# Optimization experiments

Hardware: AMD Instinct MI355X
Metric: run time of the kernel (lower is better)

Reference implementation:

```python
import jax, jax.numpy as jnp
import numpy as np

N, E, H, G, L = 100000, 200000, 32, 100, 4
NODE_IN, EDGE_IN, NGRAPH = 6, 4, 50
EPS = 1e-5

def setup_inputs() -> dict:
    key = jax.random.key(0)
    ks = jax.random.split(key, 32)
    s = 0.05
    inp = {
        "x": jax.random.normal(ks[0], (N, NODE_IN), jnp.float32),
        "edge_index": jax.random.randint(ks[1], (2, E), 0, N, jnp.int64),
        "edge_attr": jax.random.normal(ks[2], (E, EDGE_IN), jnp.float32),
        "batch": jnp.sort(jax.random.randint(ks[3], (N,), 0, NGRAPH, jnp.int64)),
        # node embedding: Linear + ReLU + BatchNorm1d
        "w_embed": jax.random.normal(ks[4], (NODE_IN, H), jnp.float32) * s,
        "b_embed": jnp.zeros((H,), jnp.float32),
        "bn_gamma": jnp.ones((H,), jnp.float32),
        "bn_beta": jnp.zeros((H,), jnp.float32),
        # NNConv layers (stacked over L): edge MLP Linear(EDGE_IN,2H)->ReLU->Linear(2H,H*H), root weight, bias
        "conv_w1": jax.random.normal(ks[5], (L, EDGE_IN, 2 * H), jnp.float32) * s,
        "conv_b1": jnp.zeros((L, 2 * H), jnp.float32),
        "conv_w2": jax.random.normal(ks[6], (L, 2 * H, H * H), jnp.float32) * s,
        "conv_b2": jnp.zeros((L, H * H), jnp.float32),
        "conv_root": jax.random.normal(ks[7], (L, H, H), jnp.float32) * s,
        "conv_bias": jnp.zeros((L, H), jnp.float32),
        # heads
        "wk_w1": jax.random.normal(ks[8], (H, H), jnp.float32) * s,
        "wk_b1": jnp.zeros((H,), jnp.float32),
        "wk_w2": jax.random.normal(ks[9], (H, 1), jnp.float32) * s,
        "wk_b2": jnp.zeros((1,), jnp.float32),
        "uj_w1": jax.random.normal(ks[10], (H, H), jnp.float32) * s,
        "uj_b1": jnp.zeros((H,), jnp.float32),
        "uj_w2": jax.random.normal(ks[11], (H, G), jnp.float32) * s,
        "uj_b2": jnp.zeros((G,), jnp.float32),
        "zk_w1": jax.random.normal(ks[12], (H, H), jnp.float32) * s,
        "zk_b1": jnp.zeros((H,), jnp.float32),
        "zk_w2": jax.random.normal(ks[13], (H, G), jnp.float32) * s,
        "zk_b2": jnp.zeros((G,), jnp.float32),
    }
    return inp

def _mlp2(h, w1, b1, w2, b2):
    return jax.nn.relu(h @ w1 + b1) @ w2 + b2

def _forward(x, edge_index, edge_attr, batch,
             w_embed, b_embed, bn_gamma, bn_beta,
             conv_w1, conv_b1, conv_w2, conv_b2, conv_root, conv_bias,
             wk_w1, wk_b1, wk_w2, wk_b2,
             uj_w1, uj_b1, uj_w2, uj_b2,
             zk_w1, zk_b1, zk_w2, zk_b2):
    src, dst = edge_index[0], edge_index[1]
    # node embed: Linear -> ReLU -> BatchNorm1d (training-mode batch stats)
    h = jax.nn.relu(x @ w_embed + b_embed)
    mu = h.mean(axis=0)
    var = ((h - mu) ** 2).mean(axis=0)  # biased, as torch BN uses for normalization
    h = (h - mu) * jax.lax.rsqrt(var + EPS) * bn_gamma + bn_beta
    # in-degree for mean aggregation
    deg = jax.ops.segment_sum(jnp.ones((E,), h.dtype), dst, num_segments=N)
    inv_deg = (1.0 / jnp.maximum(deg, 1.0))[:, None]
    for l in range(L):
        # per-edge weight matrix from edge MLP: [E, H, H]
        W = _mlp2(edge_attr, conv_w1[l], conv_b1[l], conv_w2[l], conv_b2[l]).reshape(E, H, H)
        msg = jnp.einsum('ei,eio->eo', h[src], W)  # gather + per-edge matmul
        agg = jax.ops.segment_sum(msg, dst, num_segments=N) * inv_deg  # scatter-mean
        h = jax.nn.relu(agg + h @ conv_root[l] + conv_bias[l])
    # global mean pool over graphs
    cnt = jax.ops.segment_sum(jnp.ones((N,), h.dtype), batch, num_segments=NGRAPH)
    hg = jax.ops.segment_sum(h, batch, num_segments=NGRAPH) / jnp.maximum(cnt, 1.0)[:, None]
    wk = _mlp2(hg, wk_w1, wk_b1, wk_w2, wk_b2).squeeze(-1)
    uj = _mlp2(hg, uj_w1, uj_b1, uj_w2, uj_b2)
    zk = _mlp2(hg, zk_w1, zk_b1, zk_w2, zk_b2)
    return wk, uj, zk

def reference(x, edge_index, edge_attr, batch,
              w_embed, b_embed, bn_gamma, bn_beta,
              conv_w1, conv_b1, conv_w2, conv_b2, conv_root, conv_bias,
              wk_w1, wk_b1, wk_w2, wk_b2,
              uj_w1, uj_b1, uj_w2, uj_b2,
              zk_w1, zk_b1, zk_w2, zk_b2):
    return _forward(x, edge_index, edge_attr, batch,
                    w_embed, b_embed, bn_gamma, bn_beta,
                    conv_w1, conv_b1, conv_w2, conv_b2, conv_root, conv_bias,
                    wk_w1, wk_b1, wk_w2, wk_b2,
                    uj_w1, uj_b1, uj_w2, uj_b2,
                    zk_w1, zk_b1, zk_w2, zk_b2)
```

## Files before the change

kernel.cpp:

```cpp
#include <hip/hip_runtime.h>

#define NN 100000
#define NE 200000
#define HH 32
#define NL 4
#define NGR 50
#define GOUT 100
#define NODE_IN 6
#define NEB 782

typedef __attribute__((ext_vector_type(8))) short bf16x8;
typedef __attribute__((ext_vector_type(4))) float f32x4;

__device__ __forceinline__ unsigned short bf16_rne(float x) {
    unsigned int b = __float_as_uint(x);
    b += 0x7FFFu + ((b >> 16) & 1u);
    return (unsigned short)(b >> 16);
}
__device__ __forceinline__ float bf16_f(unsigned short h) {
    return __uint_as_float(((unsigned int)h) << 16);
}

__global__ __launch_bounds__(256) void split_w2(const float* __restrict__ w2,
                                                unsigned short* __restrict__ w2h,
                                                unsigned short* __restrict__ w2l)
{
    int id = blockIdx.x * 256 + threadIdx.x;
    if (id >= NL * 64 * 1024) return;
    int l = id >> 16, rem = id & 65535;
    int k = rem >> 10, n = rem & 1023;
    float v = w2[id];
    unsigned short hi = bf16_rne(v);
    float lov = v - bf16_f(hi);
    unsigned short lo = bf16_rne(lov);
    int out = l * 65536 + n * 64 + k;
    w2h[out] = hi;
    w2l[out] = lo;
}

__global__ __launch_bounds__(256) void embed_kernel(
    const float* __restrict__ x, const float* __restrict__ w,
    const float* __restrict__ b, float* __restrict__ h0)
{
    int nid = blockIdx.x * 256 + threadIdx.x;
    if (nid >= NN) return;
    float xv[NODE_IN];
    #pragma unroll
    for (int d = 0; d < NODE_IN; ++d) xv[d] = x[nid * NODE_IN + d];
    float4* op = (float4*)(h0 + (size_t)nid * HH);
    #pragma unroll
    for (int q = 0; q < 8; ++q) {
        float4 r;
        float* rp = (float*)&r;
        #pragma unroll
        for (int u = 0; u < 4; ++u) {
            int j = q * 4 + u;
            float a = b[j];
            #pragma unroll
            for (int d = 0; d < NODE_IN; ++d) a = fmaf(xv[d], w[d * HH + j], a);
            rp[u] = fmaxf(a, 0.f);
        }
        op[q] = r;
    }
}

__global__ __launch_bounds__(256) void stats_kernel(const float* __restrict__ h0,
                                                    float* __restrict__ stats)
{
    __shared__ float ls[64];
    int tid = threadIdx.x;
    if (tid < 64) ls[tid] = 0.f;
    __syncthreads();
    float s[4] = {0.f, 0.f, 0.f, 0.f};
    float q[4] = {0.f, 0.f, 0.f, 0.f};
    const float4* h4 = (const float4*)h0;
    const int total = NN * HH / 4;
    for (int idx = blockIdx.x * 256 + tid; idx < total; idx += 128 * 256) {
        float4 v = h4[idx];
        s[0] += v.x; q[0] += v.x * v.x;
        s[1] += v.y; q[1] += v.y * v.y;
        s[2] += v.z; q[2] += v.z * v.z;
        s[3] += v.w; q[3] += v.w * v.w;
    }
    int c0 = (tid * 4) & 31;
    #pragma unroll
    for (int u = 0; u < 4; ++u) {
        atomicAdd(&ls[c0 + u], s[u]);
        atomicAdd(&ls[32 + c0 + u], q[u]);
    }
    __syncthreads();
    if (tid < 64) unsafeAtomicAdd(&stats[tid], ls[tid]);
}

__global__ __launch_bounds__(256) void degi_kernel(const int* __restrict__ ei,
                                                   int* __restrict__ degi)
{
    int e = blockIdx.x * 256 + threadIdx.x;
    if (e >= NE) return;
    atomicAdd(&degi[ei[NE + e]], 1);
}

__global__ void bn_finalize(const float* __restrict__ stats,
                            const float* __restrict__ gamma,
                            const float* __restrict__ beta,
                            float* __restrict__ bnp)
{
    int j = threadIdx.x;
    if (j >= HH) return;
    const float invn = 1.0f / (float)NN;
    float mu  = stats[j] * invn;
    float var = stats[32 + j] * invn - mu * mu;
    float rs  = 1.0f / sqrtf(var + 1e-5f);
    float sc  = rs * gamma[j];
    bnp[j]      = sc;
    bnp[32 + j] = beta[j] - mu * sc;
}

__global__ __launch_bounds__(256) void bn_apply(float* __restrict__ h,
                                                const float* __restrict__ bnp)
{
    int idx = blockIdx.x * 256 + threadIdx.x;
    if (idx >= NN * HH / 4) return;
    float4 v = ((float4*)h)[idx];
    int j = (idx * 4) & 31;
    v.x = fmaf(v.x, bnp[j + 0], bnp[32 + j + 0]);
    v.y = fmaf(v.y, bnp[j + 1], bnp[32 + j + 1]);
    v.z = fmaf(v.z, bnp[j + 2], bnp[32 + j + 2]);
    v.w = fmaf(v.w, bnp[j + 3], bnp[32 + j + 3]);
    ((float4*)h)[idx] = v;
}

__global__ __launch_bounds__(256) void scan1(const int* __restrict__ degi,
                                             int* __restrict__ rowptr,
                                             int* __restrict__ bsum)
{
    __shared__ int sd[256];
    int tid = threadIdx.x;
    int i = blockIdx.x * 256 + tid;
    int v = (i < NN) ? degi[i] : 0;
    sd[tid] = v;
    __syncthreads();
    #pragma unroll
    for (int off = 1; off < 256; off <<= 1) {
        int t = (tid >= off) ? sd[tid - off] : 0;
        __syncthreads();
        sd[tid] += t;
        __syncthreads();
    }
    if (i < NN) rowptr[i] = sd[tid] - v;
    if (tid == 255) bsum[blockIdx.x] = sd[255];
}

__global__ __launch_bounds__(512) void scan2(int* __restrict__ bsum)
{
    __shared__ int sd[512];
    int tid = threadIdx.x;
    int v = (tid < 391) ? bsum[tid] : 0;
    sd[tid] = v;
    __syncthreads();
    #pragma unroll
    for (int off = 1; off < 512; off <<= 1) {
        int t = (tid >= off) ? sd[tid - off] : 0;
        __syncthreads();
        sd[tid] += t;
        __syncthreads();
    }
    if (tid < 391) bsum[tid] = sd[tid] - v;
}

__global__ __launch_bounds__(256) void scan3(int* __restrict__ rowptr,
                                             const int* __restrict__ bsum,
                                             int* __restrict__ cursor)
{
    int i = blockIdx.x * 256 + threadIdx.x;
    if (i < NN) {
        int r = rowptr[i] + bsum[blockIdx.x];
        rowptr[i] = r;
        cursor[i] = r;
    }
    if (i == 0) rowptr[NN] = NE;
}

__global__ __launch_bounds__(256) void scatter_k(const int* __restrict__ ei,
                                                 int* __restrict__ cursor,
                                                 int* __restrict__ perm)
{
    int e = blockIdx.x * 256 + threadIdx.x;
    if (e >= NE) return;
    int d = ei[NE + e];
    int pos = atomicAdd(&cursor[d], 1);
    perm[pos] = e;
}

__global__ __launch_bounds__(256) void edge_mfma(
    const float* __restrict__ h, const int* __restrict__ ei,
    const float* __restrict__ ea, const int* __restrict__ perm,
    const float* __restrict__ w1, const float* __restrict__ b1,
    const unsigned short* __restrict__ w2h, const unsigned short* __restrict__ w2l,
    const float* __restrict__ b2, float* __restrict__ msg)
{
    __shared__ float hT[32 * 256];
    __shared__ float b2l[1024];
    __shared__ unsigned short Bh[4096];
    __shared__ unsigned short Bl[4096];

    const int tid  = threadIdx.x;
    const int lane = tid & 63;
    const int l15  = lane & 15;
    const int lg   = lane >> 4;
    const int eb   = blockIdx.x * 256;
    const int wavebase = tid & ~63;

    const unsigned int* gh = (const unsigned int*)w2h;
    const unsigned int* gl = (const unsigned int*)w2l;

    auto stage = [&](int c2) {
        #pragma unroll
        for (int q = 0; q < 2; ++q) {
            int g = q * 256 + tid;
            int n = g >> 3, j = g & 7;
            int gi = ((c2 * 64 + n) << 3) + (j ^ (n & 7));
            int lb = (q * 256 + wavebase) * 8;
            __builtin_amdgcn_global_load_lds(
                (const __attribute__((address_space(1))) unsigned int*)(gh + (size_t)gi * 4),
                (__attribute__((address_space(3))) unsigned int*)(&Bh[0] + lb), 16, 0, 0);
            __builtin_amdgcn_global_load_lds(
                (const __attribute__((address_space(1))) unsigned int*)(gl + (size_t)gi * 4),
                (__attribute__((address_space(3))) unsigned int*)(&Bl[0] + lb), 16, 0, 0);
        }
    };

    {
        int e = eb + tid;
        int pe = (e < NE) ? perm[e] : 0;
        int s  = (e < NE) ? ei[pe] : 0;
        const float4* hp = (const float4*)(h + (size_t)s * HH);
        #pragma unroll
        for (int q = 0; q < 8; ++q) {
            float4 v = hp[q];
            hT[(q * 4 + 0) * 256 + tid] = v.x;
            hT[(q * 4 + 1) * 256 + tid] = v.y;
            hT[(q * 4 + 2) * 256 + tid] = v.z;
            hT[(q * 4 + 3) * 256 + tid] = v.w;
        }
        ((float4*)b2l)[tid] = ((const float4*)b2)[tid];
    }

    bf16x8 thi[4][2], tlo[4][2];
    #pragma unroll
    for (int et = 0; et < 4; ++et) {
        int e2 = eb + wavebase + et * 16 + l15;
        bool ev = (e2 < NE);
        int pe2 = ev ? perm[e2] : 0;
        float4 eav = make_float4(0.f, 0.f, 0.f, 0.f);
        if (ev) eav = *(const float4*)(ea + (size_t)pe2 * 4);
        #pragma unroll
        for (int ks = 0; ks < 2; ++ks) {
            int k0 = ks * 32 + lg * 8;
            #pragma unroll
            for (int j = 0; j < 8; ++j) {
                float t = b1[k0 + j];
                t = fmaf(eav.x, w1[0 * 64 + k0 + j], t);
                t = fmaf(eav.y, w1[1 * 64 + k0 + j], t);
                t = fmaf(eav.z, w1[2 * 64 + k0 + j], t);
                t = fmaf(eav.w, w1[3 * 64 + k0 + j], t);
                t = ev ? fmaxf(t, 0.f) : 0.f;
                unsigned short hi = bf16_rne(t);
                float lov = t - bf16_f(hi);
                unsigned short lo = bf16_rne(lov);
                thi[et][ks][j] = (short)hi;
                tlo[et][ks][j] = (short)lo;
            }
        }
    }

    float acc0[4][4], acc1[4][4];
    #pragma unroll
    for (int et = 0; et < 4; ++et)
        #pragma unroll
        for (int r = 0; r < 4; ++r) { acc0[et][r] = 0.f; acc1[et][r] = 0.f; }

    for (int c2 = 0; c2 < 16; ++c2) {
        __syncthreads();
        stage(c2);
        __syncthreads();

        #pragma unroll
        for (int ntp = 0; ntp < 2; ++ntp) {
            const int i = c2 * 2 + ntp;
            float4 h4[4];
            #pragma unroll
            for (int et = 0; et < 4; ++et)
                h4[et] = *(const float4*)&hT[i * 256 + wavebase + et * 16 + lg * 4];
            #pragma unroll
            for (int half = 0; half < 2; ++half) {
                int nt = ntp * 2 + half;
                int nl = nt * 16 + l15;
                int swz = (nl & 7) << 4;
                const char* bhrow = (const char*)&Bh[0] + nl * 128;
                const char* blrow = (const char*)&Bl[0] + nl * 128;
                bf16x8 Bh0 = *(const bf16x8*)(bhrow + (( 0 + lg * 16) ^ swz));
                bf16x8 Bl0 = *(const bf16x8*)(blrow + (( 0 + lg * 16) ^ swz));
                bf16x8 Bh1 = *(const bf16x8*)(bhrow + ((64 + lg * 16) ^ swz));
                bf16x8 Bl1 = *(const bf16x8*)(blrow + ((64 + lg * 16) ^ swz));
                float b2v = b2l[c2 * 64 + nt * 16 + l15];
                #pragma unroll
                for (int et = 0; et < 4; ++et) {
                    f32x4 G = {0.f, 0.f, 0.f, 0.f};
                    G = __builtin_amdgcn_mfma_f32_16x16x32_bf16(thi[et][0], Bh0, G, 0, 0, 0);
                    G = __builtin_amdgcn_mfma_f32_16x16x32_bf16(tlo[et][0], Bh0, G, 0, 0, 0);
                    G = __builtin_amdgcn_mfma_f32_16x16x32_bf16(thi[et][0], Bl0, G, 0, 0, 0);
                    G = __builtin_amdgcn_mfma_f32_16x16x32_bf16(thi[et][1], Bh1, G, 0, 0, 0);
                    G = __builtin_amdgcn_mfma_f32_16x16x32_bf16(tlo[et][1], Bh1, G, 0, 0, 0);
                    G = __builtin_amdgcn_mfma_f32_16x16x32_bf16(thi[et][1], Bl1, G, 0, 0, 0);
                    if (half == 0) {
                        acc0[et][0] = fmaf(h4[et].x, G[0] + b2v, acc0[et][0]);
                        acc0[et][1] = fmaf(h4[et].y, G[1] + b2v, acc0[et][1]);
                        acc0[et][2] = fmaf(h4[et].z, G[2] + b2v, acc0[et][2]);
                        acc0[et][3] = fmaf(h4[et].w, G[3] + b2v, acc0[et][3]);
                    } else {
                        acc1[et][0] = fmaf(h4[et].x, G[0] + b2v, acc1[et][0]);
                        acc1[et][1] = fmaf(h4[et].y, G[1] + b2v, acc1[et][1]);
                        acc1[et][2] = fmaf(h4[et].z, G[2] + b2v, acc1[et][2]);
                        acc1[et][3] = fmaf(h4[et].w, G[3] + b2v, acc1[et][3]);
                    }
                }
            }
        }
    }

    #pragma unroll
    for (int et = 0; et < 4; ++et) {
        #pragma unroll
        for (int r = 0; r < 4; ++r) {
            int row = eb + wavebase + et * 16 + lg * 4 + r;
            if (row < NE) {
                msg[(size_t)row * HH + l15]      = acc0[et][r];
                msg[(size_t)row * HH + 16 + l15] = acc1[et][r];
            }
        }
    }
}

__global__ __launch_bounds__(256) void node_kernel(
    const float* __restrict__ h, const float* __restrict__ msg,
    const int* __restrict__ rowptr, const float* __restrict__ root,
    const float* __restrict__ bias, float* __restrict__ hout)
{
    int nid = blockIdx.x * 256 + threadIdx.x;
    if (nid >= NN) return;
    int j0 = rowptr[nid], j1 = rowptr[nid + 1];
    float hv[HH];
    {
        const float4* hp = (const float4*)(h + (size_t)nid * HH);
        #pragma unroll
        for (int q = 0; q < 8; ++q) {
            float4 v = hp[q];
            hv[4*q+0] = v.x; hv[4*q+1] = v.y; hv[4*q+2] = v.z; hv[4*q+3] = v.w;
        }
    }
    float acc[HH];
    #pragma unroll
    for (int o = 0; o < HH; ++o) acc[o] = bias[o];
    #pragma unroll
    for (int i = 0; i < HH; ++i) {
        float hi = hv[i];
        #pragma unroll
        for (int o = 0; o < HH; ++o) acc[o] = fmaf(hi, root[i * HH + o], acc[o]);
    }
    float s[HH];
    #pragma unroll
    for (int o = 0; o < HH; ++o) s[o] = 0.f;
    for (int j = j0; j < j1; ++j) {
        const float4* mp = (const float4*)(msg + (size_t)j * HH);
        #pragma unroll
        for (int q = 0; q < 8; ++q) {
            float4 m = mp[q];
            s[4*q+0] += m.x; s[4*q+1] += m.y; s[4*q+2] += m.z; s[4*q+3] += m.w;
        }
    }
    float inv = 1.0f / fmaxf((float)(j1 - j0), 1.0f);
    float4* op = (float4*)(hout + (size_t)nid * HH);
    #pragma unroll
    for (int q = 0; q < 8; ++q) {
        float4 r;
        r.x = fmaxf(fmaf(s[4*q+0], inv, acc[4*q+0]), 0.f);
        r.y = fmaxf(fmaf(s[4*q+1], inv, acc[4*q+1]), 0.f);
        r.z = fmaxf(fmaf(s[4*q+2], inv, acc[4*q+2]), 0.f);
        r.w = fmaxf(fmaf(s[4*q+3], inv, acc[4*q+3]), 0.f);
        op[q] = r;
    }
}

__global__ __launch_bounds__(256) void pool_kernel(
    const float* __restrict__ h, const int* __restrict__ batch,
    float* __restrict__ pool, float* __restrict__ cnt)
{
    __shared__ float lp[NGR * HH];
    __shared__ float lc[NGR];
    int tid = threadIdx.x;
    for (int i = tid; i < NGR * HH; i += 256) lp[i] = 0.f;
    if (tid < NGR) lc[tid] = 0.f;
    __syncthreads();
    int c = tid & 31, grp = tid >> 5;
    int base = blockIdx.x * 1024 + grp * 128;
    int curg = -1;
    float acc = 0.f, cn = 0.f;
    for (int s = 0; s < 128; ++s) {
        int n = base + s;
        if (n >= NN) break;
        int g = batch[n];
        if (g != curg) {
            if (curg >= 0) {
                atomicAdd(&lp[curg * HH + c], acc);
                if (c == 0) atomicAdd(&lc[curg], cn);
            }
            curg = g; acc = 0.f; cn = 0.f;
        }
        acc += h[(size_t)n * HH + c];
        cn += 1.f;
    }
    if (curg >= 0) {
        atomicAdd(&lp[curg * HH + c], acc);
        if (c == 0) atomicAdd(&lc[curg], cn);
    }
    __syncthreads();
    for (int i = tid; i < NGR * HH; i += 256)
        if (lp[i] != 0.f) unsafeAtomicAdd(&pool[i], lp[i]);
    if (tid < NGR && lc[tid] != 0.f) unsafeAtomicAdd(&cnt[tid], lc[tid]);
}

__global__ __launch_bounds__(256) void heads_kernel(
    const float* __restrict__ pool, const float* __restrict__ cnt,
    const float* __restrict__ wkw1, const float* __restrict__ wkb1,
    const float* __restrict__ wkw2, const float* __restrict__ wkb2,
    const float* __restrict__ ujw1, const float* __restrict__ ujb1,
    const float* __restrict__ ujw2, const float* __restrict__ ujb2,
    const float* __restrict__ zkw1, const float* __restrict__ zkb1,
    const float* __restrict__ zkw2, const float* __restrict__ zkb2,
    float* __restrict__ out)
{
    __shared__ float hg[NGR * HH];
    __shared__ float hid[NGR * HH];
    int tid = threadIdx.x;
    int head = blockIdx.x;
    const float *w1, *b1, *w2, *b2;
    if (head == 0)      { w1 = wkw1; b1 = wkb1; w2 = wkw2; b2 = wkb2; }
    else if (head == 1) { w1 = ujw1; b1 = ujb1; w2 = ujw2; b2 = ujb2; }
    else                { w1 = zkw1; b1 = zkb1; w2 = zkw2; b2 = zkb2; }
    for (int i = tid; i < NGR * HH; i += 256) {
        int g = i >> 5;
        hg[i] = pool[i] / fmaxf(cnt[g], 1.0f);
    }
    __syncthreads();
    for (int i = tid; i < NGR * HH; i += 256) {
        int g = i >> 5, c = i & 31;
        float a = b1[c];
        for (int j = 0; j < HH; ++j) a = fmaf(hg[g * HH + j], w1[j * HH + c], a);
        hid[i] = fmaxf(a, 0.f);
    }
    __syncthreads();
    if (head == 0) {
        if (tid < NGR) {
            float a = b2[0];
            for (int c = 0; c < HH; ++c) a = fmaf(hid[tid * HH + c], w2[c], a);
            out[tid] = a;
        }
    } else {
        float* ob = out + NGR + (head - 1) * NGR * GOUT;
        for (int i = tid; i < NGR * GOUT; i += 256) {
            int g = i / GOUT, u = i % GOUT;
            float a = b2[u];
            for (int c = 0; c < HH; ++c) a = fmaf(hid[g * HH + c], w2[c * GOUT + u], a);
            ob[i] = a;
        }
    }
}

extern "C" void kernel_launch(void* const* d_in, const int* in_sizes, int n_in,
                              void* d_out, int out_size, void* d_ws, size_t ws_size,
                              hipStream_t stream)
{
    const float* x     = (const float*)d_in[0];
    const int*   ei    = (const int*)d_in[1];
    const float* ea    = (const float*)d_in[2];
    const int*   batch = (const int*)d_in[3];
    const float* w_emb = (const float*)d_in[4];
    const float* b_emb = (const float*)d_in[5];
    const float* gamma = (const float*)d_in[6];
    const float* beta  = (const float*)d_in[7];
    const float* cw1   = (const float*)d_in[8];
    const float* cb1   = (const float*)d_in[9];
    const float* cw2   = (const float*)d_in[10];
    const float* cb2   = (const float*)d_in[11];
    const float* croot = (const float*)d_in[12];
    const float* cbias = (const float*)d_in[13];
    float* out = (float*)d_out;

    unsigned short* w2h = (unsigned short*)d_ws;
    unsigned short* w2l = w2h + 262144;
    float* msg    = (float*)(w2l + 262144);
    float* h0     = msg + (size_t)NE * HH;
    float* h1     = h0 + (size_t)NN * HH;
    int*   rowptr = (int*)(h1 + (size_t)NN * HH);
    int*   cursor = rowptr + 100004;
    int*   perm   = cursor + NN;
    int*   degi   = perm + NE;
    int*   bsum   = degi + NN;
    float* stats  = (float*)(bsum + 512);
    float* pool   = stats + 64;
    float* cnt    = pool + NGR * HH;
    float* bnp    = cnt + NGR;

    hipMemsetAsync(degi, 0, (size_t)(NN + 512 + 64 + NGR * HH + NGR) * sizeof(int), stream);

    split_w2<<<(NL * 65536) / 256, 256, 0, stream>>>(cw2, w2h, w2l);
    embed_kernel<<<(NN + 255) / 256, 256, 0, stream>>>(x, w_emb, b_emb, h0);
    stats_kernel<<<128, 256, 0, stream>>>(h0, stats);
    degi_kernel<<<NEB, 256, 0, stream>>>(ei, degi);
    bn_finalize<<<1, 32, 0, stream>>>(stats, gamma, beta, bnp);
    bn_apply<<<(NN * HH / 4 + 255) / 256, 256, 0, stream>>>(h0, bnp);

    scan1<<<391, 256, 0, stream>>>(degi, rowptr, bsum);
    scan2<<<1, 512, 0, stream>>>(bsum);
    scan3<<<391, 256, 0, stream>>>(rowptr, bsum, cursor);
    scatter_k<<<NEB, 256, 0, stream>>>(ei, cursor, perm);

    float* hc = h0;
    float* hn = h1;
    for (int l = 0; l < NL; ++l) {
        edge_mfma<<<NEB, 256, 0, stream>>>(
            hc, ei, ea, perm,
            cw1 + (size_t)l * 4 * 64, cb1 + (size_t)l * 64,
            w2h + (size_t)l * 65536, w2l + (size_t)l * 65536,
            cb2 + (size_t)l * 1024, msg);
        node_kernel<<<(NN + 255) / 256, 256, 0, stream>>>(
            hc, msg, rowptr, croot + (size_t)l * HH * HH, cbias + (size_t)l * HH, hn);
        float* t = hc; hc = hn; hn = t;
    }

    pool_kernel<<<(NN + 1023) / 1024, 256, 0, stream>>>(hc, batch, pool, cnt);
    heads_kernel<<<3, 256, 0, stream>>>(pool, cnt,
        (const float*)d_in[14], (const float*)d_in[15], (const float*)d_in[16], (const float*)d_in[17],
        (const float*)d_in[18], (const float*)d_in[19], (const float*)d_in[20], (const float*)d_in[21],
        (const float*)d_in[22], (const float*)d_in[23], (const float*)d_in[24], (const float*)d_in[25],
        out);
}
```

Measured before the change: 773.6 us.

## Load edge-MLP weights directly into registers with double-buffered prefetch

Drops the LDS staging of the split bf16 W2 tiles and the two barriers per chunk. Each wave now reads its B fragments straight from global memory (L2-resident) into registers, using a two-deep register ping-pong so loads for the next column group overlap the MFMAs of the current one. This removes barrier stalls and LDS traffic. The cost is more registers, redundant global/L2 reads across waves, and uncoalesced 16-byte loads per lane.

```diff
diff --git a/kernel.cpp b/kernel.cpp
--- a/kernel.cpp
+++ b/kernel.cpp
@@ -192,6 +192,55 @@
     perm[pos] = e;
 }
 
+#define LOADB(S, ii)                                                              \
+    {                                                                             \
+        const size_t r0 = (size_t)((ii) * 32 + l15) * 64;                         \
+        const size_t r1 = r0 + 16 * 64;                                           \
+        S##h0a = *(const bf16x8*)(wh + r0);                                       \
+        S##h0b = *(const bf16x8*)(wh + r0 + 32);                                  \
+        S##h1a = *(const bf16x8*)(wh + r1);                                       \
+        S##h1b = *(const bf16x8*)(wh + r1 + 32);                                  \
+        S##l0a = *(const bf16x8*)(wl + r0);                                       \
+        S##l0b = *(const bf16x8*)(wl + r0 + 32);                                  \
+        S##l1a = *(const bf16x8*)(wl + r1);                                       \
+        S##l1b = *(const bf16x8*)(wl + r1 + 32);                                  \
+    }
+
+#define COMPUTE(S, ii)                                                            \
+    {                                                                             \
+        float4 h4[4];                                                             \
+        _Pragma("unroll")                                                         \
+        for (int et = 0; et < 4; ++et)                                            \
+            h4[et] = *(const float4*)&hT[(ii) * 256 + wavebase + et * 16 + lg * 4];\
+        float b2v0 = b2l[(ii) * 32 + l15];                                        \
+        float b2v1 = b2l[(ii) * 32 + 16 + l15];                                   \
+        _Pragma("unroll")                                                         \
+        for (int et = 0; et < 4; ++et) {                                          \
+            f32x4 G = {0.f, 0.f, 0.f, 0.f};                                       \
+            G = __builtin_amdgcn_mfma_f32_16x16x32_bf16(thi[et][0], S##h0a, G, 0, 0, 0); \
+            G = __builtin_amdgcn_mfma_f32_16x16x32_bf16(tlo[et][0], S##h0a, G, 0, 0, 0); \
+            G = __builtin_amdgcn_mfma_f32_16x16x32_bf16(thi[et][0], S##l0a, G, 0, 0, 0); \
+            G = __builtin_amdgcn_mfma_f32_16x16x32_bf16(thi[et][1], S##h0b, G, 0, 0, 0); \
+            G = __builtin_amdgcn_mfma_f32_16x16x32_bf16(tlo[et][1], S##h0b, G, 0, 0, 0); \
+            G = __builtin_amdgcn_mfma_f32_16x16x32_bf16(thi[et][1], S##l0b, G, 0, 0, 0); \
+            acc0[et][0] = fmaf(h4[et].x, G[0] + b2v0, acc0[et][0]);               \
+            acc0[et][1] = fmaf(h4[et].y, G[1] + b2v0, acc0[et][1]);               \
+            acc0[et][2] = fmaf(h4[et].z, G[2] + b2v0, acc0[et][2]);               \
+            acc0[et][3] = fmaf(h4[et].w, G[3] + b2v0, acc0[et][3]);               \
+            f32x4 H = {0.f, 0.f, 0.f, 0.f};                                       \
+            H = __builtin_amdgcn_mfma_f32_16x16x32_bf16(thi[et][0], S##h1a, H, 0, 0, 0); \
+            H = __builtin_amdgcn_mfma_f32_16x16x32_bf16(tlo[et][0], S##h1a, H, 0, 0, 0); \
+            H = __builtin_amdgcn_mfma_f32_16x16x32_bf16(thi[et][0], S##l1a, H, 0, 0, 0); \
+            H = __builtin_amdgcn_mfma_f32_16x16x32_bf16(thi[et][1], S##h1b, H, 0, 0, 0); \
+            H = __builtin_amdgcn_mfma_f32_16x16x32_bf16(tlo[et][1], S##h1b, H, 0, 0, 0); \
+            H = __builtin_amdgcn_mfma_f32_16x16x32_bf16(thi[et][1], S##l1b, H, 0, 0, 0); \
+            acc1[et][0] = fmaf(h4[et].x, H[0] + b2v1, acc1[et][0]);               \
+            acc1[et][1] = fmaf(h4[et].y, H[1] + b2v1, acc1[et][1]);               \
+            acc1[et][2] = fmaf(h4[et].z, H[2] + b2v1, acc1[et][2]);               \
+            acc1[et][3] = fmaf(h4[et].w, H[3] + b2v1, acc1[et][3]);               \
+        }                                                                         \
+    }
+
 __global__ __launch_bounds__(256) void edge_mfma(
     const float* __restrict__ h, const int* __restrict__ ei,
     const float* __restrict__ ea, const int* __restrict__ perm,
@@ -201,8 +250,6 @@
 {
     __shared__ float hT[32 * 256];
     __shared__ float b2l[1024];
-    __shared__ unsigned short Bh[4096];
-    __shared__ unsigned short Bl[4096];
 
     const int tid  = threadIdx.x;
     const int lane = tid & 63;
@@ -211,24 +258,8 @@
     const int eb   = blockIdx.x * 256;
     const int wavebase = tid & ~63;
 
-    const unsigned int* gh = (const unsigned int*)w2h;
-    const unsigned int* gl = (const unsigned int*)w2l;
-
-    auto stage = [&](int c2) {
-        #pragma unroll
-        for (int q = 0; q < 2; ++q) {
-            int g = q * 256 + tid;
-            int n = g >> 3, j = g & 7;
-            int gi = ((c2 * 64 + n) << 3) + (j ^ (n & 7));
-            int lb = (q * 256 + wavebase) * 8;
-            __builtin_amdgcn_global_load_lds(
-                (const __attribute__((address_space(1))) unsigned int*)(gh + (size_t)gi * 4),
-                (__attribute__((address_space(3))) unsigned int*)(&Bh[0] + lb), 16, 0, 0);
-            __builtin_amdgcn_global_load_lds(
-                (const __attribute__((address_space(1))) unsigned int*)(gl + (size_t)gi * 4),
-                (__attribute__((address_space(3))) unsigned int*)(&Bl[0] + lb), 16, 0, 0);
-        }
-    };
+    const unsigned short* __restrict__ wh = w2h + lg * 8;
+    const unsigned short* __restrict__ wl = w2l + lg * 8;
 
     {
         int e = eb + tid;
@@ -280,54 +311,20 @@
         #pragma unroll
         for (int r = 0; r < 4; ++r) { acc0[et][r] = 0.f; acc1[et][r] = 0.f; }
 
-    for (int c2 = 0; c2 < 16; ++c2) {
-        __syncthreads();
-        stage(c2);
-        __syncthreads();
-
-        #pragma unroll
-        for (int ntp = 0; ntp < 2; ++ntp) {
-            const int i = c2 * 2 + ntp;
-            float4 h4[4];
-            #pragma unroll
-            for (int et = 0; et < 4; ++et)
-                h4[et] = *(const float4*)&hT[i * 256 + wavebase + et * 16 + lg * 4];
-            #pragma unroll
-            for (int half = 0; half < 2; ++half) {
-                int nt = ntp * 2 + half;
-                int nl = nt * 16 + l15;
-                int swz = (nl & 7) << 4;
-                const char* bhrow = (const char*)&Bh[0] + nl * 128;
-                const char* blrow = (const char*)&Bl[0] + nl * 128;
-                bf16x8 Bh0 = *(const bf16x8*)(bhrow + (( 0 + lg * 16) ^ swz));
-                bf16x8 Bl0 = *(const bf16x8*)(blrow + (( 0 + lg * 16) ^ swz));
-                bf16x8 Bh1 = *(const bf16x8*)(bhrow + ((64 + lg * 16) ^ swz));
-                bf16x8 Bl1 = *(const bf16x8*)(blrow + ((64 + lg * 16) ^ swz));
-                float b2v = b2l[c2 * 64 + nt * 16 + l15];
-                #pragma unroll
-                for (int et = 0; et < 4; ++et) {
-                    f32x4 G = {0.f, 0.f, 0.f, 0.f};
-                    G = __builtin_amdgcn_mfma_f32_16x16x32_bf16(thi[et][0], Bh0, G, 0, 0, 0);
-                    G = __builtin_amdgcn_mfma_f32_16x16x32_bf16(tlo[et][0], Bh0, G, 0, 0, 0);
-                    G = __builtin_amdgcn_mfma_f32_16x16x32_bf16(thi[et][0], Bl0, G, 0, 0, 0);
-                    G = __builtin_amdgcn_mfma_f32_16x16x32_bf16(thi[et][1], Bh1, G, 0, 0, 0);
-                    G = __builtin_amdgcn_mfma_f32_16x16x32_bf16(tlo[et][1], Bh1, G, 0, 0, 0);
-                    G = __builtin_amdgcn_mfma_f32_16x16x32_bf16(thi[et][1], Bl1, G, 0, 0, 0);
-                    if (half == 0) {
-                        acc0[et][0] = fmaf(h4[et].x, G[0] + b2v, acc0[et][0]);
-                        acc0[et][1] = fmaf(h4[et].y, G[1] + b2v, acc0[et][1]);
-                        acc0[et][2] = fmaf(h4[et].z, G[2] + b2v, acc0[et][2]);
-                        acc0[et][3] = fmaf(h4[et].w, G[3] + b2v, acc0[et][3]);
-                    } else {
-                        acc1[et][0] = fmaf(h4[et].x, G[0] + b2v, acc1[et][0]);
-                        acc1[et][1] = fmaf(h4[et].y, G[1] + b2v, acc1[et][1]);
-                        acc1[et][2] = fmaf(h4[et].z, G[2] + b2v, acc1[et][2]);
-                        acc1[et][3] = fmaf(h4[et].w, G[3] + b2v, acc1[et][3]);
-                    }
-                }
-            }
-        }
-    }
+    __syncthreads();
+
+    bf16x8 Ah0a, Ah0b, Ah1a, Ah1b, Al0a, Al0b, Al1a, Al1b;
+    bf16x8 Bh0a, Bh0b, Bh1a, Bh1b, Bl0a, Bl0b, Bl1a, Bl1b;
+    LOADB(A, 0);
+    for (int i = 0; i < 30; i += 2) {
+        LOADB(B, i + 1);
+        COMPUTE(A, i);
+        LOADB(A, i + 2);
+        COMPUTE(B, i + 1);
+    }
+    LOADB(B, 31);
+    COMPUTE(A, 30);
+    COMPUTE(B, 31);
 
     #pragma unroll
     for (int et = 0; et < 4; ++et) {
```

Result: slower. 902.8 us (+16.7%).
